# Kernel optimization log

Hardware: AMD Instinct MI355X
Metric: run time of the kernel (lower is better)

Reference implementation:

```python
import jax, jax.numpy as jnp
import numpy as np

B, S, H, MODES = 16, 8192, 256, 16

def setup_inputs() -> dict:
    key = jax.random.key(0)
    k1, k2, k3 = jax.random.split(key, 3)
    x = jax.random.normal(k1, (B, S, H), dtype=jnp.float32)
    # complex weights ~ 0.02 * randn (real and imag parts kept as floats)
    w_real = jax.random.normal(k2, (H, H, MODES), dtype=jnp.float32) * 0.02
    w_imag = jax.random.normal(k3, (H, H, MODES), dtype=jnp.float32) * 0.02
    return {"x": x, "w_real": w_real, "w_imag": w_imag}

def reference(x, w_real, w_imag):
    batch, seq_len, hidden = x.shape
    x_ft = jnp.fft.rfft(x, axis=1)                      # [B, F, H] complex64, F = S//2 + 1
    m = min(MODES, x_ft.shape[1])
    w = (w_real + 1j * w_imag)[:, :, :m]                # [H, K, m]
    # batched complex matmul over the kept modes (replaces per-mode loop)
    out_modes = jnp.einsum('bmh,hkm->bmk', x_ft[:, :m, :], w)
    out_ft = jnp.zeros_like(x_ft).at[:, :m, :].set(out_modes)
    y = jnp.fft.irfft(out_ft, n=seq_len, axis=1)        # [B, S, H] float32
    return jax.nn.gelu(y, approximate=False)            # torch nn.GELU default = exact erf
```

## Files before the change

kernel.cpp:

```cpp
#include <hip/hip_runtime.h>
#include <math.h>

#define BB 16
#define SS 8192
#define HH 256
#define MM 16
#define DNC 32
#define DL 128
#define SCH 16
#define SNC 129
#define QOFF (BB * MM * 2 * HH)


__global__ __launch_bounds__(256) void k_pre(const float* __restrict__ wr,
                                             const float* __restrict__ wi,
                                             float* __restrict__ T2,
                                             float* __restrict__ Wtr,
                                             float* __restrict__ Wti) {
    const int t = threadIdx.x;
    if (blockIdx.x < 256) {
        int idx = blockIdx.x * 256 + t;
        int s = idx >> 4, k = idx & 15;
        int r = (k * s) & (SS - 1);
        float th = (float)r * (6.28318530717958647692f / (float)SS);
        float sn, cn;
        sincosf(th, &sn, &cn);
        T2[s * 32 + 2 * k]     = cn;
        T2[s * 32 + 2 * k + 1] = sn;
    } else {
        __shared__ float lds[4096 + 256];
        int bid = blockIdx.x - 256;
        int h = bid & 255, y = bid >> 8;
        const float* src = (y == 0 ? wr : wi) + (size_t)h * 4096;
        float* dst = (y == 0 ? Wtr : Wti);
#pragma unroll
        for (int j = 0; j < 16; j++) {
            int i = j * 256 + t;
            lds[i + (i >> 4)] = src[i];
        }
        __syncthreads();
#pragma unroll
        for (int m = 0; m < 16; m++) {
            int i = t * 16 + m;
            dst[(size_t)m * (HH * HH) + (size_t)h * HH + t] = lds[i + (i >> 4)];
        }
    }
}

__device__ __forceinline__ float fast_gelu(float y) {
    float x  = fabsf(y) * 0.70710678118654752f;
    float t  = __builtin_amdgcn_rcpf(fmaf(0.3275911f, x, 1.0f));
    float e  = __expf(-x * x);
    float p  = fmaf(fmaf(fmaf(fmaf(1.061405429f, t, -1.453152027f), t,
                   1.421413741f), t, -0.284496736f), t, 0.254829592f) * t;
    float erfabs = fmaf(-p, e, 1.0f);
    return fmaf(0.5f * fabsf(y), erfabs, 0.5f * y);
}

__global__ __launch_bounds__(256) void k_dft(const float* __restrict__ x,
                                             const float* __restrict__ T2,
                                             float* __restrict__ Xp) {
    const int c = blockIdx.x, b = blockIdx.y, t = threadIdx.x;
    const int s0 = c * DL;
    const float* x0 = x + (size_t)b * SS * HH + (size_t)s0 * HH + t;
    const float* x1 = x0 + (size_t)(SS / 2) * HH;
    const float* tw = T2 + (size_t)s0 * 32;

    float cs[MM], sn[MM];
#pragma unroll
    for (int k = 0; k < MM; k++) { cs[k] = 0.f; sn[k] = 0.f; }

#pragma unroll 4
    for (int i = 0; i < DL; i++) {
        float xa = x0[(size_t)i * HH];
        float xb = x1[(size_t)i * HH];
        float u = xa + xb, d = xa - xb;
        const float4* t4 = (const float4*)(tw + (size_t)i * 32);
#pragma unroll
        for (int j = 0; j < 8; j++) {
            float4 tt = t4[j];
            cs[2 * j]     = fmaf(tt.x, u, cs[2 * j]);
            sn[2 * j]     = fmaf(tt.y, u, sn[2 * j]);
            cs[2 * j + 1] = fmaf(tt.z, d, cs[2 * j + 1]);
            sn[2 * j + 1] = fmaf(tt.w, d, sn[2 * j + 1]);
        }
    }

    size_t base = ((size_t)(b * DNC + c) * MM) * (2 * HH) + t;
#pragma unroll
    for (int k = 0; k < MM; k++) {
        Xp[base + (size_t)k * (2 * HH)]      = cs[k];
        Xp[base + (size_t)k * (2 * HH) + HH] = sn[k];
    }
}

__global__ __launch_bounds__(256) void k_mix(const float* __restrict__ Xp,
                                             const float* __restrict__ Wtr,
                                             const float* __restrict__ Wti,
                                             float* __restrict__ ABp) {
    const int m = blockIdx.x, b = blockIdx.y, q = blockIdx.z, t = threadIdx.x;
    const int h0 = q * 128;
    __shared__ float tmp[2][2][128];
    __shared__ float xr_s[128], xs_s[128];

    {
        int hh = t & 127, ph = t >> 7;
        float s0 = 0.f, s1 = 0.f;
        size_t base = (((size_t)b * DNC + ph * 16) * MM + m) * (2 * HH) + h0 + hh;
        const size_t ps = (size_t)MM * 2 * HH;
#pragma unroll 4
        for (int p = 0; p < 16; p++) {
            s0 += Xp[base + (size_t)p * ps];
            s1 += Xp[base + (size_t)p * ps + HH];
        }
        tmp[ph][0][hh] = s0;
        tmp[ph][1][hh] = s1;
        __syncthreads();
        if (t < 128) {
            xr_s[t] = tmp[0][0][t] + tmp[1][0][t];
            xs_s[t] = tmp[0][1][t] + tmp[1][1][t];
        }
        __syncthreads();
    }

    const float* wr_m = Wtr + (size_t)m * (HH * HH) + (size_t)h0 * HH;
    const float* wi_m = Wti + (size_t)m * (HH * HH) + (size_t)h0 * HH;
    float re = 0.f, im = 0.f;
#pragma unroll 8
    for (int hh = 0; hh < 128; hh++) {
        float a  = wr_m[(size_t)hh * HH + t];
        float bw = wi_m[(size_t)hh * HH + t];
        float xr = xr_s[hh];
        float xs = xs_s[hh];
        re = fmaf(xr, a, re);  re = fmaf(xs, bw, re);
        im = fmaf(xr, bw, im); im = fmaf(-xs, a, im);
    }
    float scale = (m == 0 ? 1.f : 2.f) / (float)SS;
    size_t o = (size_t)q * QOFF + (((size_t)b * MM + m) * 2) * HH + t;
    ABp[o]      = scale * re;
    ABp[o + HH] = -scale * im;
}

__global__ __launch_bounds__(256) void k_synth(const float* __restrict__ ABp,
                                               const float* __restrict__ T2,
                                               float* __restrict__ out) {
    const int c = blockIdx.x, b = blockIdx.y, h = threadIdx.x;
    float a[MM], bc[MM];
#pragma unroll
    for (int k = 0; k < MM; k++) {
        size_t o = (((size_t)b * MM + k) * 2) * HH + h;
        a[k]  = ABp[o]      + ABp[o + QOFF];
        bc[k] = ABp[o + HH] + ABp[o + HH + QOFF];
    }
    const int nv = (c == SNC - 1) ? 1 : SCH;
    const int v0 = c * SCH;
    float* ob = out + (size_t)b * SS * HH + h;

#pragma unroll 2
    for (int i = 0; i < nv; i++) {
        int v = v0 + i;
        const float4* tw4 = (const float4*)(T2 + (size_t)v * 32);
        float Pe = 0.f, Po = 0.f, Qe = 0.f, Qo = 0.f;
#pragma unroll
        for (int j = 0; j < 8; j++) {
            float4 t = tw4[j];
            Pe = fmaf(a[2 * j],      t.x, Pe);
            Qe = fmaf(bc[2 * j],     t.y, Qe);
            Po = fmaf(a[2 * j + 1],  t.z, Po);
            Qo = fmaf(bc[2 * j + 1], t.w, Qo);
        }
        float Pp = Pe + Po, Pm = Pe - Po, Qp = Qe + Qo, Qm = Qe - Qo;
        ob[(size_t)v * HH]                        = fast_gelu(Pp + Qp);
        ob[(size_t)(SS / 2 - v) * HH]             = fast_gelu(Pm - Qm);
        ob[(size_t)(SS / 2 + v) * HH]             = fast_gelu(Pm + Qm);
        ob[(size_t)((SS - v) & (SS - 1)) * HH]    = fast_gelu(Pp - Qp);
    }
}

extern "C" void kernel_launch(void* const* d_in, const int* in_sizes, int n_in,
                              void* d_out, int out_size, void* d_ws, size_t ws_size,
                              hipStream_t stream) {
    const float* x   = (const float*)d_in[0];
    const float* w_r = (const float*)d_in[1];
    const float* w_i = (const float*)d_in[2];
    float* out = (float*)d_out;
    float* ws  = (float*)d_ws;

    float* T2  = ws;
    float* ABp = ws + 131072;
    float* Xp  = out;
    float* Wtr = out + (size_t)16 * 1024 * 1024;
    float* Wti = out + (size_t)17 * 1024 * 1024;

    hipLaunchKernelGGL(k_pre,   dim3(768), dim3(256), 0, stream, w_r, w_i, T2, Wtr, Wti);
    hipLaunchKernelGGL(k_dft,   dim3(DNC, BB), dim3(256), 0, stream, x, T2, Xp);
    hipLaunchKernelGGL(k_mix,   dim3(MM, BB, 2), dim3(256), 0, stream, Xp, Wtr, Wti, ABp);
    hipLaunchKernelGGL(k_synth, dim3(SNC, BB), dim3(256), 0, stream, ABp, T2, out);
}
```

Before: 118.4 us.

## Retile forward DFT: stage twiddles in LDS, float4 loads, split modes across waves

The forward DFT kernel now processes 64 rows per block over 64 chunks. Each block stages its twiddle slice in shared memory. Each wave handles 4 of the 16 modes for 4 channels per lane, using float4 loads and stores on x and Xp. This increases block count for occupancy and cuts per-thread accumulator registers. The cost is that each x element is now read by all four waves (more L1/L2 traffic), and the mix kernel must reduce 32 partials instead of 16.

```diff
diff --git a/kernel.cpp b/kernel.cpp
--- a/kernel.cpp
+++ b/kernel.cpp
@@ -5,8 +5,8 @@
 #define SS 8192
 #define HH 256
 #define MM 16
-#define DNC 32
-#define DL 128
+#define DNC 64
+#define DL 64
 #define SCH 16
 #define SNC 129
 #define QOFF (BB * MM * 2 * HH)
@@ -61,36 +61,57 @@
                                              const float* __restrict__ T2,
                                              float* __restrict__ Xp) {
     const int c = blockIdx.x, b = blockIdx.y, t = threadIdx.x;
+    const int w = t >> 6, l = t & 63;
     const int s0 = c * DL;
-    const float* x0 = x + (size_t)b * SS * HH + (size_t)s0 * HH + t;
+
+    __shared__ float tw_s[DL * 32];
+    {
+        const float4* src = (const float4*)(T2 + (size_t)s0 * 32);
+        float4* dst = (float4*)tw_s;
+        dst[t * 2]     = src[t * 2];
+        dst[t * 2 + 1] = src[t * 2 + 1];
+    }
+    __syncthreads();
+
+    const float* x0 = x + (size_t)b * SS * HH + (size_t)s0 * HH + 4 * l;
     const float* x1 = x0 + (size_t)(SS / 2) * HH;
-    const float* tw = T2 + (size_t)s0 * 32;
-
-    float cs[MM], sn[MM];
-#pragma unroll
-    for (int k = 0; k < MM; k++) { cs[k] = 0.f; sn[k] = 0.f; }
+
+    float cs[4][4], sn[4][4];
+#pragma unroll
+    for (int k = 0; k < 4; k++)
+#pragma unroll
+        for (int q = 0; q < 4; q++) { cs[k][q] = 0.f; sn[k][q] = 0.f; }
 
 #pragma unroll 4
     for (int i = 0; i < DL; i++) {
-        float xa = x0[(size_t)i * HH];
-        float xb = x1[(size_t)i * HH];
-        float u = xa + xb, d = xa - xb;
-        const float4* t4 = (const float4*)(tw + (size_t)i * 32);
-#pragma unroll
-        for (int j = 0; j < 8; j++) {
-            float4 tt = t4[j];
-            cs[2 * j]     = fmaf(tt.x, u, cs[2 * j]);
-            sn[2 * j]     = fmaf(tt.y, u, sn[2 * j]);
-            cs[2 * j + 1] = fmaf(tt.z, d, cs[2 * j + 1]);
-            sn[2 * j + 1] = fmaf(tt.w, d, sn[2 * j + 1]);
-        }
-    }
-
-    size_t base = ((size_t)(b * DNC + c) * MM) * (2 * HH) + t;
-#pragma unroll
-    for (int k = 0; k < MM; k++) {
-        Xp[base + (size_t)k * (2 * HH)]      = cs[k];
-        Xp[base + (size_t)k * (2 * HH) + HH] = sn[k];
+        float4 xa = *(const float4*)(x0 + (size_t)i * HH);
+        float4 xb = *(const float4*)(x1 + (size_t)i * HH);
+        float u[4] = { xa.x + xb.x, xa.y + xb.y, xa.z + xb.z, xa.w + xb.w };
+        float d[4] = { xa.x - xb.x, xa.y - xb.y, xa.z - xb.z, xa.w - xb.w };
+        const float* tw8 = tw_s + i * 32 + w * 8;
+        float4 t0 = *(const float4*)(tw8);
+        float4 t1 = *(const float4*)(tw8 + 4);
+#pragma unroll
+        for (int q = 0; q < 4; q++) {
+            cs[0][q] = fmaf(t0.x, u[q], cs[0][q]);
+            sn[0][q] = fmaf(t0.y, u[q], sn[0][q]);
+            cs[1][q] = fmaf(t0.z, d[q], cs[1][q]);
+            sn[1][q] = fmaf(t0.w, d[q], sn[1][q]);
+            cs[2][q] = fmaf(t1.x, u[q], cs[2][q]);
+            sn[2][q] = fmaf(t1.y, u[q], sn[2][q]);
+            cs[3][q] = fmaf(t1.z, d[q], cs[3][q]);
+            sn[3][q] = fmaf(t1.w, d[q], sn[3][q]);
+        }
+    }
+
+    size_t base = ((size_t)(b * DNC + c) * MM) * (2 * HH) + 4 * l;
+#pragma unroll
+    for (int kk = 0; kk < 4; kk++) {
+        int k = 4 * w + kk;
+        *(float4*)(Xp + base + (size_t)k * (2 * HH)) =
+            make_float4(cs[kk][0], cs[kk][1], cs[kk][2], cs[kk][3]);
+        *(float4*)(Xp + base + (size_t)k * (2 * HH) + HH) =
+            make_float4(sn[kk][0], sn[kk][1], sn[kk][2], sn[kk][3]);
     }
 }
 
@@ -106,10 +127,10 @@
     {
         int hh = t & 127, ph = t >> 7;
         float s0 = 0.f, s1 = 0.f;
-        size_t base = (((size_t)b * DNC + ph * 16) * MM + m) * (2 * HH) + h0 + hh;
+        size_t base = (((size_t)b * DNC + ph * 32) * MM + m) * (2 * HH) + h0 + hh;
         const size_t ps = (size_t)MM * 2 * HH;
 #pragma unroll 4
-        for (int p = 0; p < 16; p++) {
+        for (int p = 0; p < 32; p++) {
             s0 += Xp[base + (size_t)p * ps];
             s1 += Xp[base + (size_t)p * ps + HH];
         }
```

Measured after the change: 112.2 us. -5.3%, faster.

## Drop half-period folding in DFT, double chunk count, stage twiddles in LDS

Applied to the files above, without the earlier changes.

The forward DFT kernel no longer folds x[s] and x[s+S/2] into sum/difference pairs. It now covers the full sequence with twice as many chunks (64 per batch), so the grid has twice as many blocks. The twiddle table is extended to cover all 8192 positions, and each block stages its 128-row twiddle slice in shared memory instead of reading it from global memory per iteration. The trade is twice the FMA work per input element in exchange for more parallelism and cheaper twiddle access, while the mix kernel now reduces 32 partial sums per half instead of 16.

```diff
diff --git a/kernel.cpp b/kernel.cpp
--- a/kernel.cpp
+++ b/kernel.cpp
@@ -5,7 +5,7 @@
 #define SS 8192
 #define HH 256
 #define MM 16
-#define DNC 32
+#define DNC 64
 #define DL 128
 #define SCH 16
 #define SNC 129
@@ -14,22 +14,22 @@
 
 __global__ __launch_bounds__(256) void k_pre(const float* __restrict__ wr,
                                              const float* __restrict__ wi,
-                                             float* __restrict__ T2,
+                                             float* __restrict__ T,
                                              float* __restrict__ Wtr,
                                              float* __restrict__ Wti) {
     const int t = threadIdx.x;
-    if (blockIdx.x < 256) {
+    if (blockIdx.x < 512) {
         int idx = blockIdx.x * 256 + t;
         int s = idx >> 4, k = idx & 15;
         int r = (k * s) & (SS - 1);
         float th = (float)r * (6.28318530717958647692f / (float)SS);
         float sn, cn;
         sincosf(th, &sn, &cn);
-        T2[s * 32 + 2 * k]     = cn;
-        T2[s * 32 + 2 * k + 1] = sn;
+        T[s * 32 + 2 * k]     = cn;
+        T[s * 32 + 2 * k + 1] = sn;
     } else {
         __shared__ float lds[4096 + 256];
-        int bid = blockIdx.x - 256;
+        int bid = blockIdx.x - 512;
         int h = bid & 255, y = bid >> 8;
         const float* src = (y == 0 ? wr : wi) + (size_t)h * 4096;
         float* dst = (y == 0 ? Wtr : Wti);
@@ -58,31 +58,38 @@
 }
 
 __global__ __launch_bounds__(256) void k_dft(const float* __restrict__ x,
-                                             const float* __restrict__ T2,
+                                             const float* __restrict__ T,
                                              float* __restrict__ Xp) {
     const int c = blockIdx.x, b = blockIdx.y, t = threadIdx.x;
     const int s0 = c * DL;
-    const float* x0 = x + (size_t)b * SS * HH + (size_t)s0 * HH + t;
-    const float* x1 = x0 + (size_t)(SS / 2) * HH;
-    const float* tw = T2 + (size_t)s0 * 32;
+
+    __shared__ float tws[DL * 32];
+    {
+        const float4* src = (const float4*)(T + (size_t)s0 * 32);
+        float4* dst = (float4*)tws;
+#pragma unroll
+        for (int j = 0; j < 4; j++)
+            dst[j * 256 + t] = src[j * 256 + t];
+    }
+    __syncthreads();
 
     float cs[MM], sn[MM];
 #pragma unroll
     for (int k = 0; k < MM; k++) { cs[k] = 0.f; sn[k] = 0.f; }
 
-#pragma unroll 4
+    const float* xp = x + ((size_t)b * SS + s0) * HH + t;
+
+#pragma unroll 8
     for (int i = 0; i < DL; i++) {
-        float xa = x0[(size_t)i * HH];
-        float xb = x1[(size_t)i * HH];
-        float u = xa + xb, d = xa - xb;
-        const float4* t4 = (const float4*)(tw + (size_t)i * 32);
+        float xv = xp[(size_t)i * HH];
+        const float4* tw4 = (const float4*)(tws + i * 32);
 #pragma unroll
         for (int j = 0; j < 8; j++) {
-            float4 tt = t4[j];
-            cs[2 * j]     = fmaf(tt.x, u, cs[2 * j]);
-            sn[2 * j]     = fmaf(tt.y, u, sn[2 * j]);
-            cs[2 * j + 1] = fmaf(tt.z, d, cs[2 * j + 1]);
-            sn[2 * j + 1] = fmaf(tt.w, d, sn[2 * j + 1]);
+            float4 tt = tw4[j];
+            cs[2 * j]     = fmaf(tt.x, xv, cs[2 * j]);
+            sn[2 * j]     = fmaf(tt.y, xv, sn[2 * j]);
+            cs[2 * j + 1] = fmaf(tt.z, xv, cs[2 * j + 1]);
+            sn[2 * j + 1] = fmaf(tt.w, xv, sn[2 * j + 1]);
         }
     }
 
@@ -106,10 +113,10 @@
     {
         int hh = t & 127, ph = t >> 7;
         float s0 = 0.f, s1 = 0.f;
-        size_t base = (((size_t)b * DNC + ph * 16) * MM + m) * (2 * HH) + h0 + hh;
+        size_t base = (((size_t)b * DNC + ph * 32) * MM + m) * (2 * HH) + h0 + hh;
         const size_t ps = (size_t)MM * 2 * HH;
 #pragma unroll 4
-        for (int p = 0; p < 16; p++) {
+        for (int p = 0; p < 32; p++) {
             s0 += Xp[base + (size_t)p * ps];
             s1 += Xp[base + (size_t)p * ps + HH];
         }
@@ -142,7 +149,7 @@
 }
 
 __global__ __launch_bounds__(256) void k_synth(const float* __restrict__ ABp,
-                                               const float* __restrict__ T2,
+                                               const float* __restrict__ T,
                                                float* __restrict__ out) {
     const int c = blockIdx.x, b = blockIdx.y, h = threadIdx.x;
     float a[MM], bc[MM];
@@ -159,15 +166,17 @@
 #pragma unroll 2
     for (int i = 0; i < nv; i++) {
         int v = v0 + i;
-        const float4* tw4 = (const float4*)(T2 + (size_t)v * 32);
+        const float4* tw4 = (const float4*)(T + (size_t)v * 32);
         float Pe = 0.f, Po = 0.f, Qe = 0.f, Qo = 0.f;
 #pragma unroll
         for (int j = 0; j < 8; j++) {
+            float t4x, t4y, t4z, t4w;
             float4 t = tw4[j];
-            Pe = fmaf(a[2 * j],      t.x, Pe);
-            Qe = fmaf(bc[2 * j],     t.y, Qe);
-            Po = fmaf(a[2 * j + 1],  t.z, Po);
-            Qo = fmaf(bc[2 * j + 1], t.w, Qo);
+            t4x = t.x; t4y = t.y; t4z = t.z; t4w = t.w;
+            Pe = fmaf(a[2 * j],      t4x, Pe);
+            Qe = fmaf(bc[2 * j],     t4y, Qe);
+            Po = fmaf(a[2 * j + 1],  t4z, Po);
+            Qo = fmaf(bc[2 * j + 1], t4w, Qo);
         }
         float Pp = Pe + Po, Pm = Pe - Po, Qp = Qe + Qo, Qm = Qe - Qo;
         ob[(size_t)v * HH]                        = fast_gelu(Pp + Qp);
@@ -186,14 +195,14 @@
     float* out = (float*)d_out;
     float* ws  = (float*)d_ws;
 
-    float* T2  = ws;
-    float* ABp = ws + 131072;
+    float* T   = ws;
+    float* ABp = ws + 262144;
     float* Xp  = out;
     float* Wtr = out + (size_t)16 * 1024 * 1024;
     float* Wti = out + (size_t)17 * 1024 * 1024;
 
-    hipLaunchKernelGGL(k_pre,   dim3(768), dim3(256), 0, stream, w_r, w_i, T2, Wtr, Wti);
-    hipLaunchKernelGGL(k_dft,   dim3(DNC, BB), dim3(256), 0, stream, x, T2, Xp);
+    hipLaunchKernelGGL(k_pre,   dim3(1024), dim3(256), 0, stream, w_r, w_i, T, Wtr, Wti);
+    hipLaunchKernelGGL(k_dft,   dim3(DNC, BB), dim3(256), 0, stream, x, T, Xp);
     hipLaunchKernelGGL(k_mix,   dim3(MM, BB, 2), dim3(256), 0, stream, Xp, Wtr, Wti, ABp);
-    hipLaunchKernelGGL(k_synth, dim3(SNC, BB), dim3(256), 0, stream, ABp, T2, out);
-}
+    hipLaunchKernelGGL(k_synth, dim3(SNC, BB), dim3(256), 0, stream, ABp, T, out);
+}
```

New measurement: 154.5 us. 1.3x slower.
